# Performance work log

Hardware: AMD Instinct MI355X
Metric: run time of the kernel (lower is better)

Reference implementation:

```python
import jax, jax.numpy as jnp
import numpy as np

T, B, D, H = 512, 128, 512, 512

def setup_inputs() -> dict:
    key = jax.random.key(0)
    k1, k2, k3, k4 = jax.random.split(key, 4)
    s_in = 1.0 / np.sqrt(D)
    s_h = 1.0 / np.sqrt(H)
    return {
        "x": jax.random.normal(k1, (T, B, D), dtype=jnp.float32),
        "resets": jax.random.randint(k2, (T, B), 0, 2) > 0,
        "h0": jnp.zeros((B, H), dtype=jnp.float32),  # GRUCell.initialize_carry -> zeros
        "Wi": jax.random.normal(k3, (D, 3 * H), dtype=jnp.float32) * s_in,  # [ir|iz|in]
        "bi": jnp.zeros((3 * H,), dtype=jnp.float32),
        "Wh": jax.random.normal(k4, (H, 3 * H), dtype=jnp.float32) * s_h,  # [hr|hz|hn]
        "bhn": jnp.zeros((H,), dtype=jnp.float32),
    }

def reference(x, resets, h0, Wi, bi, Wh, bhn):
    # Precompute all input-side gate projections in one big GEMM: [T,B,3H]
    xg = jnp.einsum('tbd,dk->tbk', x, Wi) + bi

    def step(h, inp):
        xg_t, reset_t = inp
        # reset masking: replace carry with fresh zero carry where episode resets
        h = jnp.where(reset_t[:, None], jnp.zeros_like(h), h)
        hg = h @ Wh  # [B,3H]
        xr, xz, xn = jnp.split(xg_t, 3, axis=-1)
        hr, hz, hn = jnp.split(hg, 3, axis=-1)
        r = jax.nn.sigmoid(xr + hr)
        z = jax.nn.sigmoid(xz + hz)
        n = jnp.tanh(xn + r * (hn + bhn))
        h_new = (1.0 - z) * n + z * h
        return h_new, h_new

    h_final, ys = jax.lax.scan(step, h0, (xg, resets))
    return h_final, ys
```

## Files before the change

kernel.cpp:

```cpp
#include <hip/hip_runtime.h>

typedef __attribute__((ext_vector_type(4))) float f32x4;
typedef __attribute__((ext_vector_type(8))) _Float16 f16x8;
typedef __attribute__((ext_vector_type(4))) _Float16 f16x4;
typedef unsigned short u16;
typedef unsigned int u32;
typedef unsigned long long u64;

#define XGCAP 34304
#define TRASH (XGCAP - 1)
#define NXG 4096

__device__ __forceinline__ float sigm(float v){ return 1.0f / (1.0f + __expf(-v)); }
__device__ __forceinline__ float tanh_fast(float v){
  v = fminf(15.0f, fmaxf(-15.0f, v));
  float e = __expf(2.0f * v);
  return (e - 1.0f) / (e + 1.0f);
}
__device__ __forceinline__ double aload(const double* p){
  return __hip_atomic_load(p, __ATOMIC_RELAXED, __HIP_MEMORY_SCOPE_AGENT);
}
__device__ __forceinline__ void astore64(u64* p, u64 v){
  __hip_atomic_store(p, v, __ATOMIC_RELAXED, __HIP_MEMORY_SCOPE_AGENT);
}
__device__ __forceinline__ u32 apoll(const u32* p){
  return __hip_atomic_load(p, __ATOMIC_RELAXED, __HIP_MEMORY_SCOPE_AGENT);
}
__device__ __forceinline__ void abump(u32* p, u32 v){
  __hip_atomic_fetch_add(p, v, __ATOMIC_RELAXED, __HIP_MEMORY_SCOPE_AGENT);
}

__global__ __launch_bounds__(512) void prep_lists(
    const void* __restrict__ resets_raw, const float* __restrict__ h0,
    u32* __restrict__ rows, u32* __restrict__ off, int* __restrict__ nlists,
    u32* __restrict__ succ, _Float16* __restrict__ hq)
{
  __shared__ u32 bitmap[2048];
  __shared__ u16 lcnt[127*128];
  __shared__ u32 cnt[520];
  __shared__ u32 offs[521];
  __shared__ u32 cur[520];
  __shared__ int is_bytes, h0nz;
  const int tid = threadIdx.x;
  const int lane = tid & 63, wave = tid >> 6;
  for (int i = tid; i < 2048; i += 512) bitmap[i] = 0;
  for (int i = tid; i < 127*128; i += 512) lcnt[i] = 0;
  for (int i = tid; i < 520; i += 512){ cnt[i] = 0; cur[i] = 0; }
  if (tid == 0){ is_bytes = 0; h0nz = 0; }
  for (int i = tid; i < 64; i += 512){ rows[65536 + i] = (2u << 16); succ[65536 + i] = TRASH; }
  __syncthreads();
  {
    const u32* w = (const u32*)resets_raw;
    int bad = 0;
    for (int i = tid; i < 4096; i += 512) bad |= (w[i] > 1u);
    if (bad) atomicOr(&is_bytes, 1);
  }
  {
    const u32* hw = (const u32*)h0;
    u32 o = 0;
    for (int i = tid; i < 65536; i += 512) o |= hw[i];
    if (o) atomicOr(&h0nz, 1);
  }
  __syncthreads();
  const bool h0zero = (h0nz == 0);
  if (is_bytes){
    const u32* wb = (const u32*)resets_raw;
    for (int i = tid; i < 16384; i += 512){
      u32 v = wb[i];
      u32 bits = ((v & 0xFFu) ? 1u : 0u) | (((v >> 8) & 0xFFu) ? 2u : 0u)
               | (((v >> 16) & 0xFFu) ? 4u : 0u) | (((v >> 24) & 0xFFu) ? 8u : 0u);
      if (bits) atomicOr(&bitmap[i >> 3], bits << ((i & 7) * 4));
    }
  } else {
    const u32* w = (const u32*)resets_raw;
    for (int r = 0; r < 128; ++r){
      u32 v = w[r * 512 + tid];
      u64 m = __ballot(v != 0u);
      if (lane == 0){
        int idx = r * 16 + wave * 2;
        bitmap[idx] = (u32)m; bitmap[idx + 1] = (u32)(m >> 32);
      }
    }
  }
  __syncthreads();
  if (tid < 128){
    const int b = tid;
    int depth = 0;
    for (int t = 0; t < 512; ++t){
      int pos = t * 128 + b;
      bool rs = (bitmap[pos >> 5] >> (pos & 31)) & 1u;
      depth = rs ? 0 : ((t == 0) ? 0 : depth + 1);
      int li = (depth == 0) ? ((rs || h0zero) ? 0 : 1) : (depth + 1);
      if (li < 127) lcnt[li*128 + b]++;
      else atomicAdd(&cnt[li], 1u);
    }
  }
  __syncthreads();
  if (tid < 127){
    const int li = tid;
    u32 s = 0;
    for (int b = 0; b < 128; ++b){
      u32 v = lcnt[li*128 + b];
      lcnt[li*128 + b] = (u16)s;
      s += v;
    }
    cnt[li] = s;
  }
  __syncthreads();
  if (tid == 0){
    u32 s = 0; int mx = 0;
    for (int i = 0; i < 520; ++i){
      offs[i] = s; s += cnt[i];
      if (cnt[i]) mx = i;
    }
    offs[520] = s;
    *nlists = mx + 1;
  }
  __syncthreads();
  for (int i = tid; i < 521; i += 512) off[i] = offs[i];
  __syncthreads();
  const u32 n0 = offs[1];
  if (tid < 128){
    const int b = tid;
    int depth = 0;
    u32 prev_p = 0;
    for (int t = 0; t < 512; ++t){
      int pos = t * 128 + b;
      bool rs = (bitmap[pos >> 5] >> (pos & 31)) & 1u;
      depth = rs ? 0 : ((t == 0) ? 0 : depth + 1);
      int li = (depth == 0) ? ((rs || h0zero) ? 0 : 1) : (depth + 1);
      u32 p;
      if (li < 127){
        u16 c = lcnt[li*128 + b];
        lcnt[li*128 + b] = (u16)(c + 1);
        p = offs[li] + c;
      } else {
        p = offs[li] + atomicAdd(&cur[li], 1u);
      }
      u32 fl = rs ? 1u : ((t == 0) ? (h0zero ? 1u : 2u) : 0u);
      rows[p] = (u32)t | ((u32)b << 9) | (fl << 16);
      succ[p] = TRASH;
      if (t > 0 && !rs) succ[prev_p] = p - n0;
      prev_p = p;
    }
  }
  __syncthreads();
  if (!h0zero){
    const u32 c1 = offs[2] - offs[1];
    for (u32 idx = tid; idx < c1 * 512u; idx += 512){
      u32 lpos = offs[1] + (idx >> 9);
      u32 c = idx & 511u;
      u32 b = (rows[lpos] >> 9) & 127u;
      hq[(size_t)(lpos - n0) * 512 + c] = (_Float16)h0[(size_t)b * 512 + c];
    }
  }
}

__global__ void prep_w(const float* __restrict__ Wi, const float* __restrict__ Wh,
                       char* __restrict__ wimg, u32* __restrict__ zflags)
{
  if (blockIdx.x < 128){
    #pragma unroll
    for (int i = 0; i < 4; ++i)
      zflags[blockIdx.x * 1024 + (int)threadIdx.x + i * 256] = 0;
  }
  __shared__ float tile[64][65];
  const int bc = blockIdx.x % 24;
  const int bk = blockIdx.x / 24;
  const int scol0 = (bc % 3) * 512 + (bc / 3) * 64;
  const int k0 = bk * 64;
  #pragma unroll
  for (int i = 0; i < 4; ++i){
    int idx = (int)threadIdx.x + i*256;
    int kk = idx >> 4, c4 = idx & 15;
    int k = k0 + kk;
    const float* src = (k < 512) ? (Wi + (size_t)k*1536 + scol0 + c4*4)
                                 : (Wh + (size_t)(k-512)*1536 + scol0 + c4*4);
    float4 v = *(const float4*)src;
    tile[kk][c4*4+0] = v.x; tile[kk][c4*4+1] = v.y;
    tile[kk][c4*4+2] = v.z; tile[kk][c4*4+3] = v.w;
  }
  __syncthreads();
  const int jb = bc / 3;
  #pragma unroll
  for (int i = 0; i < 4; ++i){
    int idx = (int)threadIdx.x + i*256;
    int cc = idx >> 4, k4 = idx & 15;
    int cimg = (bc % 3)*64 + cc;
    f16x4 c;
    c[0] = (_Float16)tile[k4*4+0][cc]; c[1] = (_Float16)tile[k4*4+1][cc];
    c[2] = (_Float16)tile[k4*4+2][cc]; c[3] = (_Float16)tile[k4*4+3][cc];
    int bby = k4*8;
    int sb = (bby & 8) | ((bby & 0x70) ^ ((cimg & 7) << 4));
    *(f16x4*)(wimg + ((size_t)(jb*16 + bk))*24576 + cimg*128 + sb) = c;
  }
}

__global__ __launch_bounds__(256, 2) void gru_fused(
    const float* __restrict__ x, const float* __restrict__ bi,
    const float* __restrict__ bhn, const char* __restrict__ wimg,
    _Float16* __restrict__ xg, _Float16* __restrict__ hq,
    const u32* __restrict__ rows, const u32* __restrict__ off,
    const int* __restrict__ nlists, const u32* __restrict__ succ,
    u32* __restrict__ hflags, u32* __restrict__ xflags,
    float* __restrict__ out)
{
  __shared__ __align__(16) char smem[40960];
  float* ys = out + 65536;
  const u32 n0 = off[1];
  const int tid = threadIdx.x;
  const int lane = tid & 63, wave = tid >> 6;
  const int nblk = (int)gridDim.x;

  int g = (int)blockIdx.x;
  while (g < NXG){
    const int tm = g >> 2, jp = g & 3;
    g += nblk;

    const float* rp[4];
    #pragma unroll
    for (int i = 0; i < 4; ++i){
      u32 e = rows[tm*64 + (tid>>4) + i*16];
      rp[i] = x + ((size_t)((e & 511u)*128u + ((e >> 9) & 127u)))*512 + (tid & 15)*4;
    }

    f32x4 acc[2][3][4];
    #pragma unroll
    for (int q = 0; q < 2; ++q)
      #pragma unroll
      for (int c = 0; c < 3; ++c)
        #pragma unroll
        for (int m = 0; m < 4; ++m) acc[q][c][m] = (f32x4){0.f,0.f,0.f,0.f};

    float4 areg[4];
    #pragma unroll
    for (int i = 0; i < 4; ++i) areg[i] = *(const float4*)(rp[i]);
    #pragma unroll
    for (int i = 0; i < 4; ++i){
      int r = (tid>>4) + i*16, bby = (tid & 15)*8;
      int sb = (bby & 8) | ((bby & 0x70) ^ ((r & 7) << 4));
      f16x4 c; c[0]=(_Float16)areg[i].x; c[1]=(_Float16)areg[i].y;
               c[2]=(_Float16)areg[i].z; c[3]=(_Float16)areg[i].w;
      *(f16x4*)(smem + r*128 + sb) = c;
    }
    __syncthreads();

    for (int kc = 0; kc < 8; ++kc){
      const int cur = kc & 1;
      if (kc < 7){
        #pragma unroll
        for (int i = 0; i < 4; ++i) areg[i] = *(const float4*)(rp[i] + (kc+1)*64);
      }
      const char* Ab = smem + cur*8192;
      #pragma unroll
      for (int kk = 0; kk < 2; ++kk){
        const int bby = kk*64 + (lane>>4)*16;
        f16x8 af[4];
        #pragma unroll
        for (int mi = 0; mi < 4; ++mi){
          int rr = mi*16 + (lane & 15);
          af[mi] = *(const f16x8*)(Ab + rr*128 + (bby ^ ((rr & 7) << 4)));
        }
        #pragma unroll
        for (int jq = 0; jq < 2; ++jq){
          const char* wp = wimg + ((size_t)((jp*2 + jq)*16 + kc))*24576;
          #pragma unroll
          for (int cls = 0; cls < 3; ++cls){
            int cc = cls*64 + wave*16 + (lane & 15);
            f16x8 wf = *(const f16x8*)(wp + cc*128 + (bby ^ ((cc & 7) << 4)));
            #pragma unroll
            for (int mi = 0; mi < 4; ++mi)
              acc[jq][cls][mi] = __builtin_amdgcn_mfma_f32_16x16x32_f16(af[mi], wf, acc[jq][cls][mi], 0, 0, 0);
          }
        }
      }
      if (kc < 7){
        char* An = smem + (cur^1)*8192;
        #pragma unroll
        for (int i = 0; i < 4; ++i){
          int r = (tid>>4) + i*16, bby = (tid & 15)*8;
          int sb = (bby & 8) | ((bby & 0x70) ^ ((r & 7) << 4));
          f16x4 c; c[0]=(_Float16)areg[i].x; c[1]=(_Float16)areg[i].y;
                   c[2]=(_Float16)areg[i].z; c[3]=(_Float16)areg[i].w;
          *(f16x4*)(An + r*128 + sb) = c;
        }
      }
      __syncthreads();
    }

    const int jloc = wave*16 + (lane & 15);
    #pragma unroll
    for (int jq = 0; jq < 2; ++jq){
      const int j = (jp*2 + jq)*64 + jloc;
      const float bir = bi[j], biz = bi[512 + j], bin = bi[1024 + j], bh = bhn[j];
      #pragma unroll
      for (int mi = 0; mi < 4; ++mi){
        #pragma unroll
        for (int rg = 0; rg < 4; ++rg){
          int r = mi*16 + (lane >> 4)*4 + rg;
          u32 e = rows[tm*64 + r];
          int tt = (int)(e & 511u), bb = (int)((e >> 9) & 127u);
          float xr = acc[jq][0][mi][rg] + bir;
          float xz = acc[jq][1][mi][rg] + biz;
          float xn = acc[jq][2][mi][rg] + bin;
          if ((e >> 16) == 1u){
            float rr = sigm(xr), zz = sigm(xz);
            float nn = tanh_fast(xn + rr*bh);
            float hv = (1.f - zz)*nn;
            ys[((size_t)(tt*128 + bb))*512 + j] = hv;
            if (tt == 511) out[(size_t)bb*512 + j] = hv;
            u32 sx = succ[tm*64 + r];
            hq[(size_t)sx*512 + j] = (_Float16)hv;
          } else {
            u32 xi = (u32)(tm*64 + r) - n0;
            if (xi >= XGCAP) xi = 0;
            _Float16* p = xg + (size_t)xi*1536 + (jp*2 + jq)*192 + jloc;
            p[0]   = (_Float16)xr;
            p[64]  = (_Float16)xz;
            p[128] = (_Float16)xn;
          }
        }
      }
    }
    __syncthreads();
    if (tid < 64){
      u32 e = rows[tm*64 + tid];
      if ((e >> 16) == 1u){
        abump(&hflags[(e & 511u)*128u + ((e >> 9) & 127u)], 2u);
      } else {
        abump(&xflags[tm*64 + tid], 1u);
      }
    }
    __syncthreads();
  }

  const int L = *nlists;
  const double* hqd = (const double*)hq;
  _Float16* hstage = (_Float16*)(smem + 32768);
  int myNext = g - NXG;
  int gt = 0;
  for (int li = 1; li < L; ++li){
    const u32 offA = off[li];
    const int nA = (int)(off[li+1] - offA);
    const int tA = (nA + 63) >> 6;
    const int nt = tA * 8;
    while (myNext < gt + nt){
      const int tile = myNext - gt;
      myNext += nblk;
      const int tm = tile >> 3, jb = tile & 7;
      const u32 rowbase = offA + (u32)tm*64u;
      const u32 xibase = rowbase - n0;
      const int mcount = min(64, nA - tm*64);
      const char* wp = wimg + ((size_t)jb*16 + 8)*24576;
      const int jloc = wave*16 + (lane & 15);

      if (wave == 0 && lane < mcount){
        u32 e = rows[rowbase + lane];
        const bool needH = ((e >> 16) == 0u);
        u32 hidx = ((e & 511u) - 1u)*128u + ((e >> 9) & 127u);
        int guard = 0;
        for (;;){
          bool ok = apoll(&xflags[rowbase + lane]) >= 4u;
          if (ok && needH) ok = apoll(&hflags[hidx]) >= 8u;
          if (ok) break;
          __builtin_amdgcn_s_sleep(1);
          if (++guard > (1 << 20)) break;
        }
      }
      __syncthreads();

      _Float16 xgp[3][4][4];
      #pragma unroll
      for (int mi = 0; mi < 4; ++mi){
        #pragma unroll
        for (int rg = 0; rg < 4; ++rg){
          u32 xi = xibase + (u32)(mi*16 + (lane >> 4)*4 + rg);
          if (xi >= XGCAP) xi = 0;
          const _Float16* p = xg + (size_t)xi*1536 + jb*192 + jloc;
          xgp[0][mi][rg] = p[0];
          xgp[1][mi][rg] = p[64];
          xgp[2][mi][rg] = p[128];
        }
      }

      f32x4 acc[3][4];
      #pragma unroll
      for (int c = 0; c < 3; ++c)
        #pragma unroll
        for (int m = 0; m < 4; ++m) acc[c][m] = (f32x4){0.f,0.f,0.f,0.f};
      float hp[4][4];
      double s0[4], s1[4], s2[4];

#define ALOAD(S, CK) do{ \
    const double* p_ = hqd + (size_t)(xibase + (u32)(tid>>2))*128 + (CK)*16 + (tid&3)*4; \
    S[0] = aload(p_); S[1] = aload(p_+1); S[2] = aload(p_+2); S[3] = aload(p_+3); }while(0)

#define AWRITE(S, CK) do{ \
    char* An_ = smem + ((CK) & 3)*8192; \
    int r_ = tid>>2; \
    _Pragma("unroll") for (int i_ = 0; i_ < 4; ++i_){ \
      int bby_ = (tid&3)*32 + i_*8; \
      int sb_ = (bby_ & 8) | ((bby_ & 0x70) ^ ((r_ & 7) << 4)); \
      *(double*)(An_ + r_*128 + sb_) = S[i_]; } }while(0)

#define COMPUTE(KC) do{ \
    const char* Ab_ = smem + ((KC) & 3)*8192; \
    _Pragma("unroll") for (int kk_ = 0; kk_ < 2; ++kk_){ \
      const int bby_ = kk_*64 + (lane>>4)*16; \
      f16x8 af_[4]; \
      _Pragma("unroll") for (int mi_ = 0; mi_ < 4; ++mi_){ \
        int rr_ = mi_*16 + (lane & 15); \
        af_[mi_] = *(const f16x8*)(Ab_ + rr_*128 + (bby_ ^ ((rr_ & 7) << 4))); } \
      _Pragma("unroll") for (int cl_ = 0; cl_ < 3; ++cl_){ \
        int cc_ = cl_*64 + wave*16 + (lane & 15); \
        f16x8 wf_ = *(const f16x8*)(wp + (size_t)(KC)*24576 + cc_*128 + (bby_ ^ ((cc_ & 7) << 4))); \
        _Pragma("unroll") for (int mi_ = 0; mi_ < 4; ++mi_) \
          acc[cl_][mi_] = __builtin_amdgcn_mfma_f32_16x16x32_f16(af_[mi_], wf_, acc[cl_][mi_], 0, 0, 0); } } \
    if ((KC) == jb){ \
      const int bb2_ = jloc*2; \
      _Pragma("unroll") for (int mi_ = 0; mi_ < 4; ++mi_) \
        _Pragma("unroll") for (int rg_ = 0; rg_ < 4; ++rg_){ \
          int r2_ = mi_*16 + (lane >> 4)*4 + rg_; \
          int sb2_ = (bb2_ & 0x0F) | ((bb2_ & 0x70) ^ ((r2_ & 7) << 4)); \
          hp[mi_][rg_] = (float)(*(const _Float16*)(Ab_ + r2_*128 + sb2_)); } } }while(0)

      ALOAD(s0, 0); ALOAD(s1, 1); ALOAD(s2, 2);
      AWRITE(s0, 0);
      __syncthreads();
      ALOAD(s0, 3); COMPUTE(0); AWRITE(s1, 1); __syncthreads();
      ALOAD(s1, 4); COMPUTE(1); AWRITE(s2, 2); __syncthreads();
      ALOAD(s2, 5); COMPUTE(2); AWRITE(s0, 3); __syncthreads();
      ALOAD(s0, 6); COMPUTE(3); AWRITE(s1, 4); __syncthreads();
      ALOAD(s1, 7); COMPUTE(4); AWRITE(s2, 5); __syncthreads();
                    COMPUTE(5); AWRITE(s0, 6); __syncthreads();
                    COMPUTE(6); AWRITE(s1, 7); __syncthreads();
                    COMPUTE(7);
#undef ALOAD
#undef AWRITE
#undef COMPUTE

      const int j = jb*64 + jloc;
      const float bh = bhn[j];
      #pragma unroll
      for (int mi = 0; mi < 4; ++mi){
        #pragma unroll
        for (int rg = 0; rg < 4; ++rg){
          int r = mi*16 + (lane >> 4)*4 + rg;
          float rr = sigm((float)xgp[0][mi][rg] + acc[0][mi][rg]);
          float zz = sigm((float)xgp[1][mi][rg] + acc[1][mi][rg]);
          float nn = tanh_fast((float)xgp[2][mi][rg] + rr*(acc[2][mi][rg] + bh));
          float hv = (1.f - zz)*nn + zz*hp[mi][rg];
          hstage[r*64 + jloc] = (_Float16)hv;
          if (r < mcount){
            u32 e = rows[rowbase + r];
            int tt = (int)(e & 511u), bb = (int)((e >> 9) & 127u);
            ys[((size_t)(tt*128 + bb))*512 + j] = hv;
            if (tt == 511) out[(size_t)bb*512 + j] = hv;
          }
        }
      }
      __syncthreads();
      {
        int row = tid >> 2;
        if (row < mcount){
          u32 sx = succ[rowbase + row];
          if (sx != TRASH){
            const u64* src = (const u64*)(hstage + row*64) + (tid & 3)*4;
            u64* dst = (u64*)hq + (size_t)sx*128 + jb*16 + (tid & 3)*4;
            astore64(dst+0, src[0]); astore64(dst+1, src[1]);
            astore64(dst+2, src[2]); astore64(dst+3, src[3]);
          }
        }
      }
      __syncthreads();
      if (tid < mcount && succ[rowbase + tid] != TRASH){
        u32 e = rows[rowbase + tid];
        abump(&hflags[(e & 511u)*128u + ((e >> 9) & 127u)], 1u);
      }
    }
    gt += nt;
  }
}

extern "C" void kernel_launch(void* const* d_in, const int* in_sizes, int n_in,
                              void* d_out, int out_size, void* d_ws, size_t ws_size,
                              hipStream_t stream)
{
  const float* x  = (const float*)d_in[0];
  const void*  resets = d_in[1];
  const float* h0 = (const float*)d_in[2];
  const float* Wi = (const float*)d_in[3];
  const float* bi = (const float*)d_in[4];
  const float* Wh = (const float*)d_in[5];
  const float* bhn= (const float*)d_in[6];
  float* out = (float*)d_out;

  char* ws = (char*)d_ws;
  u32* off    = (u32*)ws;
  int* nlists = (int*)(ws + 4096);
  u32* rows   = (u32*)(ws + 8192);
  u32* hflags = (u32*)(ws + 294912);
  u32* xflags = (u32*)(ws + 557056);
  u32* succ   = (u32*)(ws + 819200);
  char* wimg  = ws + 1081600;
  _Float16* xg = (_Float16*)(ws + 4325376);
  _Float16* hq = (_Float16*)(ws + 109707264);

  prep_lists<<<dim3(1), dim3(512), 0, stream>>>(resets, h0, rows, off, nlists, succ, hq);
  prep_w<<<dim3(384), dim3(256), 0, stream>>>(Wi, Wh, wimg, hflags);

  int perCU = 0;
  (void)hipOccupancyMaxActiveBlocksPerMultiprocessor(&perCU, gru_fused, 256, 0);
  if (perCU < 1) perCU = 1;
  int grid = perCU * 256;
  if (grid > 1024) grid = 1024;

  void* args[] = {(void*)&x, (void*)&bi, (void*)&bhn, (void*)&wimg,
                  (void*)&xg, (void*)&hq, (void*)&rows, (void*)&off,
                  (void*)&nlists, (void*)&succ, (void*)&hflags, (void*)&xflags,
                  (void*)&out};
  hipLaunchCooperativeKernel(gru_fused, dim3(grid), dim3(256), args, 0, stream);

  (void)in_sizes; (void)n_in; (void)out_size; (void)ws_size;
}
```

Before: 1.149 ms.

## Pre-convert x to swizzled fp16, DMA GEMM tiles to LDS, read h from ys

Adds a prep_x kernel that gathers x rows in list order into a pre-swizzled fp16 image. The input-projection GEMM then loads A and W tiles straight into LDS via global_load_lds into a larger double buffer, and widens tiles to 128 rows by 64 columns. The fp16 hq successor buffer and succ table are removed, so the recurrent phase reads the previous hidden state from the fp32 ys output (or h0) with atomic loads and converts it on the fly. This cuts scatter stores and per-step conversion, but doubles LDS use and adds an extra pass over x plus wider fp32 h reads.

```diff
diff --git a/kernel.cpp b/kernel.cpp
--- a/kernel.cpp
+++ b/kernel.cpp
@@ -8,7 +8,6 @@
 typedef unsigned long long u64;
 
 #define XGCAP 34304
-#define TRASH (XGCAP - 1)
 #define NXG 4096
 
 __device__ __forceinline__ float sigm(float v){ return 1.0f / (1.0f + __expf(-v)); }
@@ -17,10 +16,14 @@
   float e = __expf(2.0f * v);
   return (e - 1.0f) / (e + 1.0f);
 }
+__device__ __forceinline__ void gload16(const void* g, void* l){
+  __builtin_amdgcn_global_load_lds((const __attribute__((address_space(1))) void*)g,
+                                   (__attribute__((address_space(3))) void*)l, 16, 0, 0);
+}
 __device__ __forceinline__ double aload(const double* p){
   return __hip_atomic_load(p, __ATOMIC_RELAXED, __HIP_MEMORY_SCOPE_AGENT);
 }
-__device__ __forceinline__ void astore64(u64* p, u64 v){
+__device__ __forceinline__ void astore(float* p, float v){
   __hip_atomic_store(p, v, __ATOMIC_RELAXED, __HIP_MEMORY_SCOPE_AGENT);
 }
 __device__ __forceinline__ u32 apoll(const u32* p){
@@ -29,11 +32,11 @@
 __device__ __forceinline__ void abump(u32* p, u32 v){
   __hip_atomic_fetch_add(p, v, __ATOMIC_RELAXED, __HIP_MEMORY_SCOPE_AGENT);
 }
+__device__ __forceinline__ float2 d2f2(double d){ union{double d; float2 f;} u; u.d = d; return u.f; }
 
 __global__ __launch_bounds__(512) void prep_lists(
     const void* __restrict__ resets_raw, const float* __restrict__ h0,
-    u32* __restrict__ rows, u32* __restrict__ off, int* __restrict__ nlists,
-    u32* __restrict__ succ, _Float16* __restrict__ hq)
+    u32* __restrict__ rows, u32* __restrict__ off, int* __restrict__ nlists)
 {
   __shared__ u32 bitmap[2048];
   __shared__ u16 lcnt[127*128];
@@ -47,7 +50,7 @@
   for (int i = tid; i < 127*128; i += 512) lcnt[i] = 0;
   for (int i = tid; i < 520; i += 512){ cnt[i] = 0; cur[i] = 0; }
   if (tid == 0){ is_bytes = 0; h0nz = 0; }
-  for (int i = tid; i < 64; i += 512){ rows[65536 + i] = (2u << 16); succ[65536 + i] = TRASH; }
+  for (int i = tid; i < 64; i += 512) rows[65536 + i] = (2u << 16);
   __syncthreads();
   {
     const u32* w = (const u32*)resets_raw;
@@ -119,11 +122,9 @@
   __syncthreads();
   for (int i = tid; i < 521; i += 512) off[i] = offs[i];
   __syncthreads();
-  const u32 n0 = offs[1];
   if (tid < 128){
     const int b = tid;
     int depth = 0;
-    u32 prev_p = 0;
     for (int t = 0; t < 512; ++t){
       int pos = t * 128 + b;
       bool rs = (bitmap[pos >> 5] >> (pos & 31)) & 1u;
@@ -139,19 +140,6 @@
       }
       u32 fl = rs ? 1u : ((t == 0) ? (h0zero ? 1u : 2u) : 0u);
       rows[p] = (u32)t | ((u32)b << 9) | (fl << 16);
-      succ[p] = TRASH;
-      if (t > 0 && !rs) succ[prev_p] = p - n0;
-      prev_p = p;
-    }
-  }
-  __syncthreads();
-  if (!h0zero){
-    const u32 c1 = offs[2] - offs[1];
-    for (u32 idx = tid; idx < c1 * 512u; idx += 512){
-      u32 lpos = offs[1] + (idx >> 9);
-      u32 c = idx & 511u;
-      u32 b = (rows[lpos] >> 9) & 127u;
-      hq[(size_t)(lpos - n0) * 512 + c] = (_Float16)h0[(size_t)b * 512 + c];
     }
   }
 }
@@ -196,16 +184,37 @@
   }
 }
 
+__global__ __launch_bounds__(256) void prep_x(
+    const float* __restrict__ x, const u32* __restrict__ rows,
+    char* __restrict__ xq)
+{
+  const int tid = threadIdx.x;
+  const u32 lpos = blockIdx.x * 16 + (tid >> 4);
+  const u32 e = rows[lpos];
+  const float* src = x + ((size_t)((e & 511u)*128u + ((e >> 9) & 127u)))*512;
+  const int lane16 = tid & 15;
+  char* dst = xq + (size_t)lpos * 1024;
+  const int swzr = ((int)lpos & 7) << 4;
+  #pragma unroll
+  for (int it = 0; it < 8; ++it){
+    float4 v = *(const float4*)(src + it*64 + lane16*4);
+    f16x4 c; c[0]=(_Float16)v.x; c[1]=(_Float16)v.y;
+             c[2]=(_Float16)v.z; c[3]=(_Float16)v.w;
+    int bby = lane16 * 8;
+    int sb = (bby & 8) | ((bby & 0x70) ^ swzr);
+    *(f16x4*)(dst + it*128 + sb) = c;
+  }
+}
+
 __global__ __launch_bounds__(256, 2) void gru_fused(
-    const float* __restrict__ x, const float* __restrict__ bi,
+    const char* __restrict__ xq, const float* __restrict__ bi,
     const float* __restrict__ bhn, const char* __restrict__ wimg,
-    _Float16* __restrict__ xg, _Float16* __restrict__ hq,
+    const float* __restrict__ h0, _Float16* __restrict__ xg,
     const u32* __restrict__ rows, const u32* __restrict__ off,
-    const int* __restrict__ nlists, const u32* __restrict__ succ,
-    u32* __restrict__ hflags, u32* __restrict__ xflags,
-    float* __restrict__ out)
+    const int* __restrict__ nlists, u32* __restrict__ hflags,
+    u32* __restrict__ xflags, float* __restrict__ out)
 {
-  __shared__ __align__(16) char smem[40960];
+  __shared__ __align__(16) char smem[81920];
   float* ys = out + 65536;
   const u32 n0 = off[1];
   const int tid = threadIdx.x;
@@ -214,129 +223,97 @@
 
   int g = (int)blockIdx.x;
   while (g < NXG){
-    const int tm = g >> 2, jp = g & 3;
+    const int tm = g >> 3, jb = g & 7;
     g += nblk;
-
-    const float* rp[4];
+    const char* asrc = xq + (size_t)tm * 131072;
+    const char* wsrc = wimg + ((size_t)jb * 16) * 24576;
+
+    f32x4 acc[3][8];
     #pragma unroll
-    for (int i = 0; i < 4; ++i){
-      u32 e = rows[tm*64 + (tid>>4) + i*16];
-      rp[i] = x + ((size_t)((e & 511u)*128u + ((e >> 9) & 127u)))*512 + (tid & 15)*4;
-    }
-
-    f32x4 acc[2][3][4];
-    #pragma unroll
-    for (int q = 0; q < 2; ++q)
-      #pragma unroll
-      for (int c = 0; c < 3; ++c)
-        #pragma unroll
-        for (int m = 0; m < 4; ++m) acc[q][c][m] = (f32x4){0.f,0.f,0.f,0.f};
-
-    float4 areg[4];
-    #pragma unroll
-    for (int i = 0; i < 4; ++i) areg[i] = *(const float4*)(rp[i]);
-    #pragma unroll
-    for (int i = 0; i < 4; ++i){
-      int r = (tid>>4) + i*16, bby = (tid & 15)*8;
-      int sb = (bby & 8) | ((bby & 0x70) ^ ((r & 7) << 4));
-      f16x4 c; c[0]=(_Float16)areg[i].x; c[1]=(_Float16)areg[i].y;
-               c[2]=(_Float16)areg[i].z; c[3]=(_Float16)areg[i].w;
-      *(f16x4*)(smem + r*128 + sb) = c;
-    }
+    for (int c = 0; c < 3; ++c)
+      #pragma unroll
+      for (int m = 0; m < 8; ++m) acc[c][m] = (f32x4){0.f,0.f,0.f,0.f};
+
+#define DMA_A(KC, BUF) do{ \
+    char* l_ = smem + (BUF)*16384 + wave*4096; \
+    const char* g_ = asrc + (size_t)(wave*32 + (lane>>3))*1024 + (KC)*128 + (lane&7)*16; \
+    _Pragma("unroll") for (int i_ = 0; i_ < 4; ++i_) \
+      gload16(g_ + i_*8192, l_ + i_*1024); }while(0)
+#define DMA_W(KC, BUF) do{ \
+    char* l_ = smem + 32768 + (BUF)*24576 + wave*6144; \
+    const char* g_ = wsrc + (size_t)(KC)*24576 + wave*6144 + lane*16; \
+    _Pragma("unroll") for (int i_ = 0; i_ < 6; ++i_) \
+      gload16(g_ + i_*1024, l_ + i_*1024); }while(0)
+
+    DMA_A(0, 0); DMA_W(0, 0);
     __syncthreads();
-
     for (int kc = 0; kc < 8; ++kc){
       const int cur = kc & 1;
-      if (kc < 7){
-        #pragma unroll
-        for (int i = 0; i < 4; ++i) areg[i] = *(const float4*)(rp[i] + (kc+1)*64);
-      }
-      const char* Ab = smem + cur*8192;
+      if (kc < 7){ DMA_A(kc+1, cur^1); DMA_W(kc+1, cur^1); }
+      const char* Ab = smem + cur*16384;
+      const char* Wb = smem + 32768 + cur*24576;
       #pragma unroll
       for (int kk = 0; kk < 2; ++kk){
         const int bby = kk*64 + (lane>>4)*16;
-        f16x8 af[4];
+        f16x8 af[8];
         #pragma unroll
-        for (int mi = 0; mi < 4; ++mi){
+        for (int mi = 0; mi < 8; ++mi){
           int rr = mi*16 + (lane & 15);
           af[mi] = *(const f16x8*)(Ab + rr*128 + (bby ^ ((rr & 7) << 4)));
         }
         #pragma unroll
-        for (int jq = 0; jq < 2; ++jq){
-          const char* wp = wimg + ((size_t)((jp*2 + jq)*16 + kc))*24576;
+        for (int cls = 0; cls < 3; ++cls){
+          int cc = cls*64 + wave*16 + (lane & 15);
+          f16x8 wf = *(const f16x8*)(Wb + cc*128 + (bby ^ ((cc & 7) << 4)));
           #pragma unroll
-          for (int cls = 0; cls < 3; ++cls){
-            int cc = cls*64 + wave*16 + (lane & 15);
-            f16x8 wf = *(const f16x8*)(wp + cc*128 + (bby ^ ((cc & 7) << 4)));
-            #pragma unroll
-            for (int mi = 0; mi < 4; ++mi)
-              acc[jq][cls][mi] = __builtin_amdgcn_mfma_f32_16x16x32_f16(af[mi], wf, acc[jq][cls][mi], 0, 0, 0);
-          }
+          for (int mi = 0; mi < 8; ++mi)
+            acc[cls][mi] = __builtin_amdgcn_mfma_f32_16x16x32_f16(af[mi], wf, acc[cls][mi], 0, 0, 0);
         }
       }
-      if (kc < 7){
-        char* An = smem + (cur^1)*8192;
-        #pragma unroll
-        for (int i = 0; i < 4; ++i){
-          int r = (tid>>4) + i*16, bby = (tid & 15)*8;
-          int sb = (bby & 8) | ((bby & 0x70) ^ ((r & 7) << 4));
-          f16x4 c; c[0]=(_Float16)areg[i].x; c[1]=(_Float16)areg[i].y;
-                   c[2]=(_Float16)areg[i].z; c[3]=(_Float16)areg[i].w;
-          *(f16x4*)(An + r*128 + sb) = c;
+      __syncthreads();
+    }
+#undef DMA_A
+#undef DMA_W
+
+    const int jloc = wave*16 + (lane & 15);
+    const int j = jb*64 + jloc;
+    const float bir = bi[j], biz = bi[512 + j], bin = bi[1024 + j], bh = bhn[j];
+    #pragma unroll
+    for (int mi = 0; mi < 8; ++mi){
+      #pragma unroll
+      for (int rg = 0; rg < 4; ++rg){
+        int r = mi*16 + (lane >> 4)*4 + rg;
+        u32 e = rows[tm*128 + r];
+        int tt = (int)(e & 511u), bb = (int)((e >> 9) & 127u);
+        float xr = acc[0][mi][rg] + bir;
+        float xz = acc[1][mi][rg] + biz;
+        float xn = acc[2][mi][rg] + bin;
+        if ((e >> 16) == 1u){
+          float rr = sigm(xr), zz = sigm(xz);
+          float nn = tanh_fast(xn + rr*bh);
+          float hv = (1.f - zz)*nn;
+          ys[((size_t)(tt*128 + bb))*512 + j] = hv;
+          if (tt == 511) out[(size_t)bb*512 + j] = hv;
+        } else {
+          u32 xi = (u32)(tm*128 + r) - n0;
+          if (xi >= XGCAP) xi = 0;
+          _Float16* p = xg + (size_t)xi*1536 + jb*192 + jloc;
+          p[0]   = (_Float16)xr;
+          p[64]  = (_Float16)xz;
+          p[128] = (_Float16)xn;
         }
       }
-      __syncthreads();
-    }
-
-    const int jloc = wave*16 + (lane & 15);
-    #pragma unroll
-    for (int jq = 0; jq < 2; ++jq){
-      const int j = (jp*2 + jq)*64 + jloc;
-      const float bir = bi[j], biz = bi[512 + j], bin = bi[1024 + j], bh = bhn[j];
-      #pragma unroll
-      for (int mi = 0; mi < 4; ++mi){
-        #pragma unroll
-        for (int rg = 0; rg < 4; ++rg){
-          int r = mi*16 + (lane >> 4)*4 + rg;
-          u32 e = rows[tm*64 + r];
-          int tt = (int)(e & 511u), bb = (int)((e >> 9) & 127u);
-          float xr = acc[jq][0][mi][rg] + bir;
-          float xz = acc[jq][1][mi][rg] + biz;
-          float xn = acc[jq][2][mi][rg] + bin;
-          if ((e >> 16) == 1u){
-            float rr = sigm(xr), zz = sigm(xz);
-            float nn = tanh_fast(xn + rr*bh);
-            float hv = (1.f - zz)*nn;
-            ys[((size_t)(tt*128 + bb))*512 + j] = hv;
-            if (tt == 511) out[(size_t)bb*512 + j] = hv;
-            u32 sx = succ[tm*64 + r];
-            hq[(size_t)sx*512 + j] = (_Float16)hv;
-          } else {
-            u32 xi = (u32)(tm*64 + r) - n0;
-            if (xi >= XGCAP) xi = 0;
-            _Float16* p = xg + (size_t)xi*1536 + (jp*2 + jq)*192 + jloc;
-            p[0]   = (_Float16)xr;
-            p[64]  = (_Float16)xz;
-            p[128] = (_Float16)xn;
-          }
-        }
-      }
     }
     __syncthreads();
-    if (tid < 64){
-      u32 e = rows[tm*64 + tid];
-      if ((e >> 16) == 1u){
-        abump(&hflags[(e & 511u)*128u + ((e >> 9) & 127u)], 2u);
-      } else {
-        abump(&xflags[tm*64 + tid], 1u);
-      }
+    if (tid < 128){
+      u32 e = rows[tm*128 + tid];
+      if ((e >> 16) == 1u) abump(&hflags[(e & 511u)*128u + ((e >> 9) & 127u)], 1u);
+      else                 abump(&xflags[tm*128 + tid], 1u);
     }
     __syncthreads();
   }
 
   const int L = *nlists;
-  const double* hqd = (const double*)hq;
-  _Float16* hstage = (_Float16*)(smem + 32768);
   int myNext = g - NXG;
   int gt = 0;
   for (int li = 1; li < L; ++li){
@@ -360,7 +337,7 @@
         u32 hidx = ((e & 511u) - 1u)*128u + ((e >> 9) & 127u);
         int guard = 0;
         for (;;){
-          bool ok = apoll(&xflags[rowbase + lane]) >= 4u;
+          bool ok = apoll(&xflags[rowbase + lane]) >= 8u;
           if (ok && needH) ok = apoll(&hflags[hidx]) >= 8u;
           if (ok) break;
           __builtin_amdgcn_s_sleep(1);
@@ -368,6 +345,16 @@
         }
       }
       __syncthreads();
+
+      const float* rp[4];
+      #pragma unroll
+      for (int i = 0; i < 4; ++i){
+        u32 e = rows[rowbase + (tid>>4) + i*16];
+        int tt = (int)(e & 511u), bb = (int)((e >> 9) & 127u);
+        const float* base = ((e >> 16) == 0u) ? (ys + ((size_t)((tt-1)*128 + bb))*512)
+                                              : (h0 + (size_t)bb*512);
+        rp[i] = base + (tid & 15)*4;
+      }
 
       _Float16 xgp[3][4][4];
       #pragma unroll
@@ -389,19 +376,22 @@
         #pragma unroll
         for (int m = 0; m < 4; ++m) acc[c][m] = (f32x4){0.f,0.f,0.f,0.f};
       float hp[4][4];
-      double s0[4], s1[4], s2[4];
+      double s0[4][2], s1[4][2], s2[4][2];
 
 #define ALOAD(S, CK) do{ \
-    const double* p_ = hqd + (size_t)(xibase + (u32)(tid>>2))*128 + (CK)*16 + (tid&3)*4; \
-    S[0] = aload(p_); S[1] = aload(p_+1); S[2] = aload(p_+2); S[3] = aload(p_+3); }while(0)
+    _Pragma("unroll") for (int i_ = 0; i_ < 4; ++i_){ \
+      const double* p_ = (const double*)(rp[i_] + (CK)*64); \
+      S[i_][0] = aload(p_); S[i_][1] = aload(p_ + 1); } }while(0)
 
 #define AWRITE(S, CK) do{ \
     char* An_ = smem + ((CK) & 3)*8192; \
-    int r_ = tid>>2; \
     _Pragma("unroll") for (int i_ = 0; i_ < 4; ++i_){ \
-      int bby_ = (tid&3)*32 + i_*8; \
+      float2 u0_ = d2f2(S[i_][0]), u1_ = d2f2(S[i_][1]); \
+      int r_ = (tid>>4) + i_*16, bby_ = (tid & 15)*8; \
       int sb_ = (bby_ & 8) | ((bby_ & 0x70) ^ ((r_ & 7) << 4)); \
-      *(double*)(An_ + r_*128 + sb_) = S[i_]; } }while(0)
+      f16x4 c_; c_[0]=(_Float16)u0_.x; c_[1]=(_Float16)u0_.y; \
+                c_[2]=(_Float16)u1_.x; c_[3]=(_Float16)u1_.y; \
+      *(f16x4*)(An_ + r_*128 + sb_) = c_; } }while(0)
 
 #define COMPUTE(KC) do{ \
     const char* Ab_ = smem + ((KC) & 3)*8192; \
@@ -446,34 +436,20 @@
         #pragma unroll
         for (int rg = 0; rg < 4; ++rg){
           int r = mi*16 + (lane >> 4)*4 + rg;
-          float rr = sigm((float)xgp[0][mi][rg] + acc[0][mi][rg]);
-          float zz = sigm((float)xgp[1][mi][rg] + acc[1][mi][rg]);
-          float nn = tanh_fast((float)xgp[2][mi][rg] + rr*(acc[2][mi][rg] + bh));
-          float hv = (1.f - zz)*nn + zz*hp[mi][rg];
-          hstage[r*64 + jloc] = (_Float16)hv;
           if (r < mcount){
             u32 e = rows[rowbase + r];
             int tt = (int)(e & 511u), bb = (int)((e >> 9) & 127u);
-            ys[((size_t)(tt*128 + bb))*512 + j] = hv;
+            float rr = sigm((float)xgp[0][mi][rg] + acc[0][mi][rg]);
+            float zz = sigm((float)xgp[1][mi][rg] + acc[1][mi][rg]);
+            float nn = tanh_fast((float)xgp[2][mi][rg] + rr*(acc[2][mi][rg] + bh));
+            float hv = (1.f - zz)*nn + zz*hp[mi][rg];
+            astore(&ys[((size_t)(tt*128 + bb))*512 + j], hv);
             if (tt == 511) out[(size_t)bb*512 + j] = hv;
           }
         }
       }
       __syncthreads();
-      {
-        int row = tid >> 2;
-        if (row < mcount){
-          u32 sx = succ[rowbase + row];
-          if (sx != TRASH){
-            const u64* src = (const u64*)(hstage + row*64) + (tid & 3)*4;
-            u64* dst = (u64*)hq + (size_t)sx*128 + jb*16 + (tid & 3)*4;
-            astore64(dst+0, src[0]); astore64(dst+1, src[1]);
-            astore64(dst+2, src[2]); astore64(dst+3, src[3]);
-          }
-        }
-      }
-      __syncthreads();
-      if (tid < mcount && succ[rowbase + tid] != TRASH){
+      if (tid < mcount){
         u32 e = rows[rowbase + tid];
         abump(&hflags[(e & 511u)*128u + ((e >> 9) & 127u)], 1u);
       }
@@ -501,13 +477,13 @@
   u32* rows   = (u32*)(ws + 8192);
   u32* hflags = (u32*)(ws + 294912);
   u32* xflags = (u32*)(ws + 557056);
-  u32* succ   = (u32*)(ws + 819200);
-  char* wimg  = ws + 1081600;
-  _Float16* xg = (_Float16*)(ws + 4325376);
-  _Float16* hq = (_Float16*)(ws + 109707264);
-
-  prep_lists<<<dim3(1), dim3(512), 0, stream>>>(resets, h0, rows, off, nlists, succ, hq);
+  char* wimg  = ws + 819200;
+  char* xq    = ws + 4194304;
+  _Float16* xg = (_Float16*)(ws + 71303168);
+
+  prep_lists<<<dim3(1), dim3(512), 0, stream>>>(resets, h0, rows, off, nlists);
   prep_w<<<dim3(384), dim3(256), 0, stream>>>(Wi, Wh, wimg, hflags);
+  prep_x<<<dim3(4096), dim3(256), 0, stream>>>(x, rows, xq);
 
   int perCU = 0;
   (void)hipOccupancyMaxActiveBlocksPerMultiprocessor(&perCU, gru_fused, 256, 0);
@@ -515,10 +491,9 @@
   int grid = perCU * 256;
   if (grid > 1024) grid = 1024;
 
-  void* args[] = {(void*)&x, (void*)&bi, (void*)&bhn, (void*)&wimg,
-                  (void*)&xg, (void*)&hq, (void*)&rows, (void*)&off,
-                  (void*)&nlists, (void*)&succ, (void*)&hflags, (void*)&xflags,
-                  (void*)&out};
+  void* args[] = {(void*)&xq, (void*)&bi, (void*)&bhn, (void*)&wimg,
+                  (void*)&h0, (void*)&xg, (void*)&rows, (void*)&off,
+                  (void*)&nlists, (void*)&hflags, (void*)&xflags, (void*)&out};
   hipLaunchCooperativeKernel(gru_fused, dim3(grid), dim3(256), args, 0, stream);
 
   (void)in_sizes; (void)n_in; (void)out_size; (void)ws_size;
```

Measured after the change: 1.011 ms. -12.1%, faster.
